# Optimization experiments

Measured on AMD Instinct MI355X. Metric: run time of the kernel, lower is better.

The kernel has to match this reference:

```python
import jax, jax.numpy as jnp
import numpy as np

V, E, H = 4996, 64, 64  # vocab, embed dim, GRU units per direction
B, S = 128, 512


def _gru_scan(xw, mask, U, b_r):
    """Masked GRU (Keras reset_after=True semantics).
    xw:   [S, B, 3H] precomputed input projections (x@W + b_input)
    mask: [S, B, 1] bool; masked steps carry previous state (Keras masking).
    U:    [H, 3H] recurrent kernel, b_r: [3H] recurrent bias.
    Returns per-step hidden states [S, B, H].
    """
    def step(h, inp):
        xw_t, m = inp
        rec = h @ U + b_r                                   # [B, 3H]
        z = jax.nn.sigmoid(xw_t[:, :H] + rec[:, :H])        # update gate
        r = jax.nn.sigmoid(xw_t[:, H:2*H] + rec[:, H:2*H])  # reset gate
        hh = jnp.tanh(xw_t[:, 2*H:] + r * rec[:, 2*H:])     # candidate
        h_new = z * h + (1.0 - z) * hh
        h = jnp.where(m, h_new, h)                          # skip masked steps
        return h, h

    h0 = jnp.zeros((xw.shape[1], H), xw.dtype)
    _, ys = jax.lax.scan(step, h0, (xw, mask))
    return ys


def setup_inputs() -> dict:
    key = jax.random.key(0)
    ks = jax.random.split(key, 12)
    sc = 0.1
    inp = {
        "inputs": jax.random.randint(ks[0], (B, S), 0, V),
        "emb": jax.random.normal(ks[1], (V, E), jnp.float32) * sc,
        "Wf": jax.random.normal(ks[2], (E, 3 * H), jnp.float32) * sc,
        "Uf": jax.random.normal(ks[3], (H, 3 * H), jnp.float32) * sc,
        "bif": jnp.zeros((3 * H,), jnp.float32),
        "brf": jnp.zeros((3 * H,), jnp.float32),
        "Wb": jax.random.normal(ks[4], (E, 3 * H), jnp.float32) * sc,
        "Ub": jax.random.normal(ks[5], (H, 3 * H), jnp.float32) * sc,
        "bib": jnp.zeros((3 * H,), jnp.float32),
        "brb": jnp.zeros((3 * H,), jnp.float32),
        "w1": jax.random.normal(ks[6], (2 * H, 1), jnp.float32) * sc,
        "b1": jnp.zeros((1,), jnp.float32),
        "w2": jax.random.normal(ks[7], (2 * H, 1), jnp.float32) * sc,
        "b2": jnp.zeros((1,), jnp.float32),
    }
    return inp


def reference(inputs, emb, Wf, Uf, bif, brf, Wb, Ub, bib, brb, w1, b1, w2, b2):
    mask = (inputs != 0)                       # [B, S] mask_zero semantics
    x = emb[inputs]                            # [B, S, E]
    xt = jnp.swapaxes(x, 0, 1)                 # [S, B, E] time-major
    m = jnp.swapaxes(mask, 0, 1)[:, :, None]   # [S, B, 1]

    # forward direction
    fwd = _gru_scan(xt @ Wf + bif, m, Uf, brf)                 # [S, B, H]
    # backward direction: reverse time, scan, reverse back
    bwd = _gru_scan((xt @ Wb + bib)[::-1], m[::-1], Ub, brb)[::-1]

    gru_out = jnp.swapaxes(jnp.concatenate([fwd, bwd], axis=-1), 0, 1)  # [B, S, 2H]
    x1 = jax.nn.sigmoid(gru_out @ w1 + b1)     # [B, S, 1]
    x2 = jax.nn.sigmoid(gru_out @ w2 + b2)     # [B, S, 1]
    return x1, x2, gru_out
```

## Files before the change

kernel.cpp:

```cpp
#include <hip/hip_runtime.h>
#include <hip/hip_bf16.h>
#include <hip/hip_fp16.h>

#define B_  128
#define S_  512
#define H_  64
#define E_  64
#define G3  192
#define V_  4996
#define VCHUNK 32

typedef float f32x2 __attribute__((ext_vector_type(2)));
typedef float f32x4 __attribute__((ext_vector_type(4)));
typedef unsigned int u32;
typedef u32 u32x4 __attribute__((ext_vector_type(4)));
typedef _Float16 f16;
typedef f16 f16x2 __attribute__((ext_vector_type(2)));

__device__ __forceinline__ float sigmoidf_(float x) {
    return 1.0f / (1.0f + __expf(-x));
}

__device__ __forceinline__ float tanh_fast(float x) {
    x = fminf(fmaxf(x, -15.0f), 15.0f);
    const float e = __expf(2.0f * x);
    return (e - 1.0f) / (e + 1.0f);
}

__device__ __forceinline__ float fdot2_(u32 a, u32 b, float c) {
#if __has_builtin(__builtin_amdgcn_fdot2)
    return __builtin_amdgcn_fdot2(__builtin_bit_cast(f16x2, a),
                                  __builtin_bit_cast(f16x2, b), c, false);
#else
    const f16x2 av = __builtin_bit_cast(f16x2, a);
    const f16x2 bv = __builtin_bit_cast(f16x2, b);
    return fmaf((float)av.x, (float)bv.x, fmaf((float)av.y, (float)bv.y, c));
#endif
}

__global__ __launch_bounds__(192) void proj_kernel(
    const float* __restrict__ emb,
    const float* __restrict__ Wf, const float* __restrict__ bif,
    const float* __restrict__ Wb, const float* __restrict__ bib,
    float* __restrict__ proj)
{
    const int dir = blockIdx.y;
    const float* W  = dir ? Wb  : Wf;
    const float* bi = dir ? bib : bif;
    const int v0 = blockIdx.x * VCHUNK;
    const int j  = threadIdx.x;
    const int nrows = min(VCHUNK, V_ - v0);

    __shared__ __align__(16) float s_e[VCHUNK * E_];
    for (int i = j; i < nrows * E_; i += 192) s_e[i] = emb[(size_t)v0 * E_ + i];

    float wcol[E_];
    #pragma unroll
    for (int e = 0; e < E_; ++e) wcol[e] = W[e * G3 + j];
    const float bij = bi[j];
    __syncthreads();

    for (int r = 0; r < nrows; ++r) {
        const float4* x4 = (const float4*)(s_e + r * E_);
        float a0 = 0.f, a1 = 0.f, a2 = 0.f, a3 = 0.f;
        #pragma unroll
        for (int e4 = 0; e4 < 16; e4 += 4) {
            float4 h0 = x4[e4], h1 = x4[e4+1], h2 = x4[e4+2], h3 = x4[e4+3];
            a0 = fmaf(h0.x, wcol[4*e4+ 0], a0); a0 = fmaf(h0.y, wcol[4*e4+ 1], a0);
            a0 = fmaf(h0.z, wcol[4*e4+ 2], a0); a0 = fmaf(h0.w, wcol[4*e4+ 3], a0);
            a1 = fmaf(h1.x, wcol[4*e4+ 4], a1); a1 = fmaf(h1.y, wcol[4*e4+ 5], a1);
            a1 = fmaf(h1.z, wcol[4*e4+ 6], a1); a1 = fmaf(h1.w, wcol[4*e4+ 7], a1);
            a2 = fmaf(h2.x, wcol[4*e4+ 8], a2); a2 = fmaf(h2.y, wcol[4*e4+ 9], a2);
            a2 = fmaf(h2.z, wcol[4*e4+10], a2); a2 = fmaf(h2.w, wcol[4*e4+11], a2);
            a3 = fmaf(h3.x, wcol[4*e4+12], a3); a3 = fmaf(h3.y, wcol[4*e4+13], a3);
            a3 = fmaf(h3.z, wcol[4*e4+14], a3); a3 = fmaf(h3.w, wcol[4*e4+15], a3);
        }
        proj[((size_t)dir * V_ + v0 + r) * G3 + j] = ((a0 + a1) + (a2 + a3)) + bij;
    }
}

__global__ void upack_kernel(const float* __restrict__ Uf,
                             const float* __restrict__ Ub,
                             u32* __restrict__ Uh)
{
    const int dir = blockIdx.x;
    const float* U = dir ? Ub : Uf;
    u32* o = Uh + (size_t)dir * G3 * 32;
    for (int k = threadIdx.x; k < G3 * 32; k += blockDim.x) {
        const int j = k >> 5, kk = k & 31;
        f16x2 p;
        p.x = (f16)U[(2 * kk    ) * G3 + j];
        p.y = (f16)U[(2 * kk + 1) * G3 + j];
        o[(size_t)j * 32 + kk] = __builtin_bit_cast(u32, p);
    }
}

__global__ __launch_bounds__(64)
__attribute__((amdgpu_waves_per_eu(1, 1)))
void gru_scan7(
    const int*   __restrict__ inputs,
    const float* __restrict__ proj,
    const u32*   __restrict__ Uh,
    const float* __restrict__ brf, const float* __restrict__ brb,
    float* __restrict__ gru_out)
{
    const int b   = blockIdx.x >> 1;
    const int dir = blockIdx.x & 1;
    const int u   = threadIdx.x;

    const float* eproj = proj + (size_t)dir * V_ * G3;
    const float* br    = dir ? brb : brf;

    __shared__ int s_idx[S_];
    __shared__ __align__(16) f16 s_h[H_];

    for (int t = u; t < S_; t += 64) s_idx[t] = inputs[b * S_ + t];
    s_h[u] = (f16)0.0f;
    __builtin_amdgcn_wave_barrier();

    u32x4 wz[8], wr[8], wc[8];
    {
        const u32x4* pz = (const u32x4*)(Uh + ((size_t)dir * G3 + u      ) * 32);
        const u32x4* pr = (const u32x4*)(Uh + ((size_t)dir * G3 + u + 64 ) * 32);
        const u32x4* pc = (const u32x4*)(Uh + ((size_t)dir * G3 + u + 128) * 32);
        #pragma unroll
        for (int k = 0; k < 8; ++k) { wz[k] = pz[k]; wr[k] = pr[k]; wc[k] = pc[k]; }
        #pragma unroll
        for (int k = 0; k < 8; ++k) {
            asm volatile("" : "+v"(wz[k]));
            asm volatile("" : "+v"(wr[k]));
            asm volatile("" : "+v"(wc[k]));
        }
    }
    const float br0 = br[u], br1 = br[u + 64], br2 = br[u + 128];
    float hprev = 0.0f;

    float xw0[4], xw1[4], xw2[4];
    int   tokp[4];
    auto pref = [&](int tstep, int p) {
        if (tstep < S_) {
            const int tt = dir ? (S_ - 1 - tstep) : tstep;
            int tk = s_idx[tt];
            tk = __builtin_amdgcn_readfirstlane(tk);
            tokp[p] = tk;
            const float* rowp = eproj + (size_t)tk * G3;
            xw0[p] = rowp[u];
            xw1[p] = rowp[u + 64];
            xw2[p] = rowp[u + 128];
        }
    };
    #pragma unroll
    for (int p = 0; p < 4; ++p) pref(p, p);

    float* outb = gru_out + (size_t)b * S_ * (2 * H_) + dir * H_ + u;

    for (int t = 0; t < S_; t += 4) {
        #pragma unroll
        for (int p = 0; p < 4; ++p) {
            const int tstep = t + p;
            const int tok   = tokp[p];
            const float x0 = xw0[p], x1 = xw1[p], x2 = xw2[p];

            const u32x4* h8 = (const u32x4*)s_h;
            float az[4] = {0,0,0,0}, ar_[4] = {0,0,0,0}, ac_[4] = {0,0,0,0};
            #pragma unroll
            for (int k = 0; k < 8; ++k) {
                const u32x4 hv = h8[k];
                const u32x4 vz = wz[k], vr = wr[k], vc = wc[k];
                az[0]  = fdot2_(hv.x, vz.x, az[0]);
                az[1]  = fdot2_(hv.y, vz.y, az[1]);
                az[2]  = fdot2_(hv.z, vz.z, az[2]);
                az[3]  = fdot2_(hv.w, vz.w, az[3]);
                ar_[0] = fdot2_(hv.x, vr.x, ar_[0]);
                ar_[1] = fdot2_(hv.y, vr.y, ar_[1]);
                ar_[2] = fdot2_(hv.z, vr.z, ar_[2]);
                ar_[3] = fdot2_(hv.w, vr.w, ar_[3]);
                ac_[0] = fdot2_(hv.x, vc.x, ac_[0]);
                ac_[1] = fdot2_(hv.y, vc.y, ac_[1]);
                ac_[2] = fdot2_(hv.z, vc.z, ac_[2]);
                ac_[3] = fdot2_(hv.w, vc.w, ac_[3]);
            }
            const float d0 = ((az[0]  + az[1])  + (az[2]  + az[3]))  + br0;
            const float d1 = ((ar_[0] + ar_[1]) + (ar_[2] + ar_[3])) + br1;
            const float d2 = ((ac_[0] + ac_[1]) + (ac_[2] + ac_[3])) + br2;

            const float z    = sigmoidf_(x0 + d0);
            const float r    = sigmoidf_(x1 + d1);
            const float hh   = tanh_fast(x2 + r * d2);
            const float hnew = z * hprev + (1.0f - z) * hh;
            const float res  = (tok != 0) ? hnew : hprev;
            hprev = res;

            s_h[u] = (f16)res;
            __builtin_amdgcn_wave_barrier();

            const int tt = dir ? (S_ - 1 - tstep) : tstep;
            outb[(size_t)tt * (2 * H_)] = res;

            pref(tstep + 4, p);
        }
    }
}

__global__ __launch_bounds__(256) void head_kernel(
    const float* __restrict__ gru,
    const float* __restrict__ w1, const float* __restrict__ b1,
    const float* __restrict__ w2, const float* __restrict__ b2,
    float* __restrict__ x1, float* __restrict__ x2)
{
    __shared__ __align__(16) float s_w1[2 * H_];
    __shared__ __align__(16) float s_w2[2 * H_];
    const int tid = threadIdx.x;
    if (tid < 2 * H_)      s_w1[tid]          = w1[tid];
    else                   s_w2[tid - 2 * H_] = w2[tid - 2 * H_];
    __syncthreads();

    const int i = blockIdx.x * 256 + tid;
    const float4* g4 = (const float4*)(gru + (size_t)i * (2 * H_));
    float a1 = b1[0], a2 = b2[0];
    #pragma unroll
    for (int k = 0; k < (2 * H_) / 4; ++k) {
        const float4 v  = g4[k];
        const float4 q1 = ((const float4*)s_w1)[k];
        const float4 q2 = ((const float4*)s_w2)[k];
        a1 += v.x * q1.x + v.y * q1.y + v.z * q1.z + v.w * q1.w;
        a2 += v.x * q2.x + v.y * q2.y + v.z * q2.z + v.w * q2.w;
    }
    x1[i] = sigmoidf_(a1);
    x2[i] = sigmoidf_(a2);
}

extern "C" void kernel_launch(void* const* d_in, const int* in_sizes, int n_in,
                              void* d_out, int out_size, void* d_ws, size_t ws_size,
                              hipStream_t stream) {
    (void)in_sizes; (void)n_in; (void)ws_size; (void)out_size;

    const int*   inputs = (const int*)  d_in[0];
    const float* emb    = (const float*)d_in[1];
    const float* Wf     = (const float*)d_in[2];
    const float* Uf     = (const float*)d_in[3];
    const float* bif    = (const float*)d_in[4];
    const float* brf    = (const float*)d_in[5];
    const float* Wb     = (const float*)d_in[6];
    const float* Ub     = (const float*)d_in[7];
    const float* bib    = (const float*)d_in[8];
    const float* brb    = (const float*)d_in[9];
    const float* w1     = (const float*)d_in[10];
    const float* b1     = (const float*)d_in[11];
    const float* w2     = (const float*)d_in[12];
    const float* b2     = (const float*)d_in[13];

    float* out = (float*)d_out;
    float* x1  = out;
    float* x2  = out + (size_t)B_ * S_;
    float* gru = out + (size_t)2 * B_ * S_;

    float* proj = (float*)d_ws;
    u32*   Uh   = (u32*)(proj + (size_t)2 * V_ * G3);

    proj_kernel<<<dim3((V_ + VCHUNK - 1) / VCHUNK, 2), 192, 0, stream>>>(
        emb, Wf, bif, Wb, bib, proj);
    upack_kernel<<<2, 256, 0, stream>>>(Uf, Ub, Uh);

    gru_scan7<<<B_ * 2, 64, 0, stream>>>(inputs, proj, Uh, brf, brb, gru);

    head_kernel<<<(B_ * S_) / 256, 256, 0, stream>>>(gru, w1, b1, w2, b2, x1, x2);
}
```

Measured before the change: 269.1 us.

## Stage GRU input projections in double-buffered LDS chunks and use fast rcp/exp activations

Replaces the 4-deep per-step register prefetch of gathered projection rows with chunked staging. Each chunk of 16 timesteps is loaded as vectorized f32x4 loads into registers while the current chunk computes, then written to a double-buffered LDS area. Tokens are stored pre-reversed for the backward direction. Sigmoid and tanh now use hardware rcp/exp2 builtins, with tanh rewritten without clamping and the state update folded into FMAs. This aims to move global-load latency off the serial recurrence critical path, at the cost of more LDS, 12 live f32x4 registers, and slightly looser activation accuracy.

```diff
diff --git a/kernel.cpp b/kernel.cpp
--- a/kernel.cpp
+++ b/kernel.cpp
@@ -9,22 +9,35 @@
 #define G3  192
 #define V_  4996
 #define VCHUNK 32
-
-typedef float f32x2 __attribute__((ext_vector_type(2)));
+#define CHUNK  16
+#define NCHUNK (S_ / CHUNK)
+#define STOK  (S_ + CHUNK)
+
 typedef float f32x4 __attribute__((ext_vector_type(4)));
 typedef unsigned int u32;
 typedef u32 u32x4 __attribute__((ext_vector_type(4)));
 typedef _Float16 f16;
 typedef f16 f16x2 __attribute__((ext_vector_type(2)));
 
+__device__ __forceinline__ float fast_rcp(float x) {
+#if __has_builtin(__builtin_amdgcn_rcpf)
+    return __builtin_amdgcn_rcpf(x);
+#else
+    return 1.0f / x;
+#endif
+}
+__device__ __forceinline__ float fast_exp(float x) {
+#if __has_builtin(__builtin_amdgcn_exp2f)
+    return __builtin_amdgcn_exp2f(x * 1.44269504f);
+#else
+    return __expf(x);
+#endif
+}
 __device__ __forceinline__ float sigmoidf_(float x) {
-    return 1.0f / (1.0f + __expf(-x));
-}
-
+    return fast_rcp(1.0f + fast_exp(-x));
+}
 __device__ __forceinline__ float tanh_fast(float x) {
-    x = fminf(fmaxf(x, -15.0f), 15.0f);
-    const float e = __expf(2.0f * x);
-    return (e - 1.0f) / (e + 1.0f);
+    return 1.0f - 2.0f * fast_rcp(1.0f + fast_exp(2.0f * x));
 }
 
 __device__ __forceinline__ float fdot2_(u32 a, u32 b, float c) {
@@ -97,7 +110,7 @@
 
 __global__ __launch_bounds__(64)
 __attribute__((amdgpu_waves_per_eu(1, 1)))
-void gru_scan7(
+void gru_scan9(
     const int*   __restrict__ inputs,
     const float* __restrict__ proj,
     const u32*   __restrict__ Uh,
@@ -111,10 +124,13 @@
     const float* eproj = proj + (size_t)dir * V_ * G3;
     const float* br    = dir ? brb : brf;
 
-    __shared__ int s_idx[S_];
-    __shared__ __align__(16) f16 s_h[H_];
-
-    for (int t = u; t < S_; t += 64) s_idx[t] = inputs[b * S_ + t];
+    __shared__ __align__(16) int   s_tok[STOK];
+    __shared__ __align__(16) f16   s_h[H_];
+    __shared__ __align__(16) float s_xw[2][CHUNK * G3];
+
+    for (int t = u; t < S_; t += 64)
+        s_tok[t] = inputs[b * S_ + (dir ? (S_ - 1 - t) : t)];
+    for (int t = S_ + u; t < STOK; t += 64) s_tok[t] = 0;
     s_h[u] = (f16)0.0f;
     __builtin_amdgcn_wave_barrier();
 
@@ -135,31 +151,43 @@
     const float br0 = br[u], br1 = br[u + 64], br2 = br[u + 128];
     float hprev = 0.0f;
 
-    float xw0[4], xw1[4], xw2[4];
-    int   tokp[4];
-    auto pref = [&](int tstep, int p) {
-        if (tstep < S_) {
-            const int tt = dir ? (S_ - 1 - tstep) : tstep;
-            int tk = s_idx[tt];
-            tk = __builtin_amdgcn_readfirstlane(tk);
-            tokp[p] = tk;
-            const float* rowp = eproj + (size_t)tk * G3;
-            xw0[p] = rowp[u];
-            xw1[p] = rowp[u + 64];
-            xw2[p] = rowp[u + 128];
+    f32x4 ld[12];
+    auto stage_issue = [&](int baseStep) {
+        #pragma unroll
+        for (int i = 0; i < 12; ++i) {
+            const int idx = i * 64 + u;
+            const int row = idx / 48;
+            const int off = idx - row * 48;
+            const int tk  = s_tok[baseStep + row];
+            ld[i] = *(const f32x4*)(eproj + (size_t)tk * G3 + off * 4);
         }
     };
-    #pragma unroll
-    for (int p = 0; p < 4; ++p) pref(p, p);
+    auto stage_write = [&](int nbuf) {
+        #pragma unroll
+        for (int i = 0; i < 12; ++i) {
+            const int idx = i * 64 + u;
+            *(f32x4*)(&s_xw[nbuf][idx * 4]) = ld[i];
+        }
+    };
+
+    stage_issue(0);
+    stage_write(0);
+    __builtin_amdgcn_wave_barrier();
 
     float* outb = gru_out + (size_t)b * S_ * (2 * H_) + dir * H_ + u;
 
-    for (int t = 0; t < S_; t += 4) {
-        #pragma unroll
-        for (int p = 0; p < 4; ++p) {
-            const int tstep = t + p;
-            const int tok   = tokp[p];
-            const float x0 = xw0[p], x1 = xw1[p], x2 = xw2[p];
+    for (int c = 0; c < NCHUNK; ++c) {
+        const int buf = c & 1;
+        stage_issue((c + 1) * CHUNK);
+
+        #pragma unroll 1
+        for (int t0 = 0; t0 < CHUNK; ++t0) {
+            const int t = c * CHUNK + t0;
+
+            const int   tok = s_tok[t];
+            const float x0  = s_xw[buf][t0 * G3 + u];
+            const float x1  = s_xw[buf][t0 * G3 + u + 64];
+            const float x2  = s_xw[buf][t0 * G3 + u + 128];
 
             const u32x4* h8 = (const u32x4*)s_h;
             float az[4] = {0,0,0,0}, ar_[4] = {0,0,0,0}, ac_[4] = {0,0,0,0};
@@ -186,19 +214,20 @@
 
             const float z    = sigmoidf_(x0 + d0);
             const float r    = sigmoidf_(x1 + d1);
-            const float hh   = tanh_fast(x2 + r * d2);
-            const float hnew = z * hprev + (1.0f - z) * hh;
+            const float hh   = tanh_fast(fmaf(r, d2, x2));
+            const float hnew = fmaf(z, hprev - hh, hh);
             const float res  = (tok != 0) ? hnew : hprev;
             hprev = res;
 
             s_h[u] = (f16)res;
             __builtin_amdgcn_wave_barrier();
 
-            const int tt = dir ? (S_ - 1 - tstep) : tstep;
+            const int tt = dir ? (S_ - 1 - t) : t;
             outb[(size_t)tt * (2 * H_)] = res;
-
-            pref(tstep + 4, p);
-        }
+        }
+
+        stage_write(buf ^ 1);
+        __builtin_amdgcn_wave_barrier();
     }
 }
 
@@ -226,8 +255,8 @@
         a1 += v.x * q1.x + v.y * q1.y + v.z * q1.z + v.w * q1.w;
         a2 += v.x * q2.x + v.y * q2.y + v.z * q2.z + v.w * q2.w;
     }
-    x1[i] = sigmoidf_(a1);
-    x2[i] = sigmoidf_(a2);
+    x1[i] = 1.0f / (1.0f + __expf(-a1));
+    x2[i] = 1.0f / (1.0f + __expf(-a2));
 }
 
 extern "C" void kernel_launch(void* const* d_in, const int* in_sizes, int n_in,
@@ -262,7 +291,7 @@
         emb, Wf, bif, Wb, bib, proj);
     upack_kernel<<<2, 256, 0, stream>>>(Uf, Ub, Uh);
 
-    gru_scan7<<<B_ * 2, 64, 0, stream>>>(inputs, proj, Uh, brf, brb, gru);
+    gru_scan9<<<B_ * 2, 64, 0, stream>>>(inputs, proj, Uh, brf, brb, gru);
 
     head_kernel<<<(B_ * S_) / 256, 256, 0, stream>>>(gru, w1, b1, w2, b2, x1, x2);
 }
```

New measurement: 235.8 us. -12.4%, faster.
